# Performance work log

Measured on AMD Instinct MI355X. Metric: run time of the kernel, lower is better.

The kernel has to match this reference:

```python
import jax, jax.numpy as jnp
from jax import lax
import numpy as np

QMIN, QMAX = -127.0, 127.0
STRIDE = (1, 1)
PADDING = ((1, 1), (1, 1))
DILATION = (1, 1)
DN = ('NCHW', 'OIHW', 'NCHW')


def _quantize_x(x, scale_x):
    # symmetric static per-tensor int8 quantization
    return jnp.clip(jnp.round(x / scale_x), QMIN, QMAX)


def _quantize_w(w):
    # symmetric dynamic per-output-channel int8 quantization
    scale_w = jnp.max(jnp.abs(w), axis=(1, 2, 3), keepdims=True) / QMAX  # [O,1,1,1]
    q_w = jnp.clip(jnp.round(w / scale_w), QMIN, QMAX)
    return q_w, scale_w


def setup_inputs() -> dict:
    key = jax.random.key(0)
    kx, kw, kb = jax.random.split(key, 3)
    B, C, H, W = 32, 128, 56, 56
    O, kH, kW = 256, 3, 3
    x = jax.random.normal(kx, (B, C, H, W), jnp.float32)
    weight = jax.random.normal(kw, (O, C, kH, kW), jnp.float32) * 0.05
    bias = jax.random.normal(kb, (O,), jnp.float32)
    scale_x = jnp.asarray(0.02, jnp.float32)  # static per-tensor scale buffer
    # exact int8 product lookup table: lut[a+127, b+127] = a*b
    v = np.arange(-127, 128, dtype=np.int32)
    lut = jnp.asarray(v[:, None] * v[None, :])
    return {"x": x, "weight": weight, "bias": bias, "scale_x": scale_x, "lut": lut}


def reference(x, weight, bias, scale_x, lut):
    # lut holds the exact int8 product table, so bgemm_int8(q_x, q_w, lut) is an
    # exact integer GEMM; im2col + bGEMM == conv of quantized tensors.
    q_x = _quantize_x(x, scale_x)            # [B,C,H,W] integer-valued fp32
    q_w, scale_w = _quantize_w(weight)       # [O,C,kH,kW], [O,1,1,1]
    acc = lax.conv_general_dilated(
        q_x, q_w, STRIDE, PADDING, rhs_dilation=DILATION, dimension_numbers=DN
    )                                        # [B,O,OH,OW] integer-valued accumulator
    out = acc * scale_x * scale_w.reshape(1, -1, 1, 1)  # per-channel dequant
    return out + bias.reshape(1, -1, 1, 1)
```

## Files before the change

### kernel.cpp

```cpp
#include <hip/hip_runtime.h>


#define BATCH 32
#define CIN   128
#define HH    56
#define WW    56
#define OCH   256

typedef __attribute__((ext_vector_type(4))) int int4v;
typedef __attribute__((ext_vector_type(2))) long longx2;

#define QX_BYTES (32 * 56 * 56 * 128)
#define QW_BYTES (256 * 1152)
#define WS_NEEDED (QX_BYTES + QW_BYTES + 1024)

__device__ __forceinline__ void gload_lds16(const void* g, void* l) {
  __builtin_amdgcn_global_load_lds(
      (const __attribute__((address_space(1))) unsigned int*)g,
      (__attribute__((address_space(3))) unsigned int*)l, 16, 0, 0);
}

__global__ __launch_bounds__(256) void quant_w_kernel(
    const float* __restrict__ w, const float* __restrict__ sxp,
    char* __restrict__ qwf, float* __restrict__ alpha) {
  __shared__ float wf[1152];
  __shared__ float red[256];
  const int o = blockIdx.x;
  const int tid = threadIdx.x;
  const float* wrow = w + (size_t)o * 1152;
  float m = 0.f;
  for (int i = tid; i < 288; i += 256) {
    const float4 v = ((const float4*)wrow)[i];
    ((float4*)wf)[i] = v;
    m = fmaxf(m, fmaxf(fmaxf(fabsf(v.x), fabsf(v.y)),
                       fmaxf(fabsf(v.z), fabsf(v.w))));
  }
  red[tid] = m;
  __syncthreads();
  for (int s = 128; s > 0; s >>= 1) {
    if (tid < s) red[tid] = fmaxf(red[tid], red[tid + s]);
    __syncthreads();
  }
  const float sc = red[0] / 127.0f;
  if (tid == 0) alpha[o] = sc * sxp[0];
  if (tid < 36) {
    const int r = tid >> 2, c04 = tid & 3;
    const int og = o >> 5, t = (o >> 4) & 1, l16 = o & 15;
    unsigned int* base = (unsigned int*)(qwf + (size_t)og * 36864 +
                                         (size_t)(r * 4 + c04) * 1024);
#pragma unroll
    for (int quad = 0; quad < 4; ++quad) {
#pragma unroll
      for (int half = 0; half < 2; ++half) {
        unsigned int pk = 0;
#pragma unroll
        for (int k = 0; k < 4; ++k) {
          const int c = c04 * 32 + quad * 8 + half * 4 + k;
          const int q =
              (int)fminf(127.f, fmaxf(-127.f, rintf(wf[c * 9 + r] / sc)));
          pk |= ((unsigned int)(q & 255)) << (8 * k);
        }
        base[(l16 * 4 + quad) * 4 + t * 2 + half] = pk;
      }
    }
  }
}

__global__ __launch_bounds__(256) void quant_x_kernel(
    const float* __restrict__ x, const float* __restrict__ sxp,
    unsigned int* __restrict__ qxp) {
  __shared__ char ldsA[128 * 60];
  const int row = blockIdx.x;
  const int b = row / 56, h = row % 56;
  const float sx = sxp[0];
  for (int i = threadIdx.x; i < 1792; i += 256) {
    const int c = i / 14, f = i % 14;
    const float4 v =
        *(const float4*)(x + (((size_t)b * 128 + c) * 56 + h) * 56 + 4 * f);
    unsigned int pk;
    pk  = (unsigned int)((int)fminf(127.f, fmaxf(-127.f, rintf(v.x / sx))) & 255);
    pk |= ((unsigned int)((int)fminf(127.f, fmaxf(-127.f, rintf(v.y / sx))) & 255)) << 8;
    pk |= ((unsigned int)((int)fminf(127.f, fmaxf(-127.f, rintf(v.z / sx))) & 255)) << 16;
    pk |= ((unsigned int)((int)fminf(127.f, fmaxf(-127.f, rintf(v.w / sx))) & 255)) << 24;
    *(unsigned int*)(ldsA + c * 60 + 4 * f) = pk;
  }
  __syncthreads();
  unsigned int* orow = qxp + (size_t)row * 56 * 32;
  for (int i = threadIdx.x; i < 1792; i += 256) {
    const int w = i >> 5, jd = i & 31;
    const int c0 = (jd ^ (((w + 1) & 15) << 1)) << 2;
    unsigned int pk = 0;
#pragma unroll
    for (int k = 0; k < 4; ++k)
      pk |= ((unsigned int)(unsigned char)ldsA[(c0 + k) * 60 + w]) << (8 * k);
    orow[i] = pk;
  }
}

#define XSLAB 8448

__global__ __launch_bounds__(256, 4) void conv_kernel(
    const char* __restrict__ qxp, const char* __restrict__ qwf,
    const float* __restrict__ alpha, const float* __restrict__ bias,
    float* __restrict__ out) {
  __shared__ __attribute__((aligned(16))) char Xs8[3 * XSLAB];

  const int id = blockIdx.x;
  const int xcd = id & 7;
  int kk = id >> 3;
  const int yy = (kk >= 224) ? 1 : 0;
  kk -= yy * 224;
  const int bi = xcd * 224 + kk;
  const int b  = bi / 56;
  const int oh = bi % 56;
  const int o0 = yy * 128;
  const int tid = threadIdx.x;
  const int wave = tid >> 6, lane = tid & 63;
  const int l16 = lane & 15, quad = lane >> 4;

  int m_r[4], n_r[4];
  {
    int4v zz = {0, 0, 0, 0};
    long a1 = 0, b1 = 0, a2 = 0, b2 = 0;
    if (quad == 0) {
      a1 = 1L;
      b1 = (long)(l16 + 1);
      a2 = (long)(l16 + 1);
      b2 = 1L;
    }
    int4v d1 = __builtin_amdgcn_mfma_i32_16x16x32_i8(a1, b1, zz, 0, 0, 0);
    int4v d2 = __builtin_amdgcn_mfma_i32_16x16x32_i8(a2, b2, zz, 0, 0, 0);
#pragma unroll
    for (int r = 0; r < 4; ++r) {
      n_r[r] = (d1[r] - 1) & 15;
      m_r[r] = (d2[r] - 1) & 15;
    }
  }

  const longx2* wb2 = (const longx2*)(qwf + (size_t)(yy * 4 + wave) * 36864) +
                      (l16 * 4 + quad);
  longx2 ap[2][4];
#pragma unroll
  for (int c04 = 0; c04 < 4; ++c04) ap[0][c04] = wb2[(size_t)c04 * 64];

  for (int kh = 0; kh < 3; ++kh) {
    const int ih = oh - 1 + kh;
    char* slab = Xs8 + kh * XSLAB;
    if (ih >= 0 && ih < HH) {
      const char* src = qxp + ((size_t)b * 56 + ih) * 7168;
      for (int i = tid; i < 448; i += 256)
        gload_lds16(src + i * 16, slab + 128 + i * 16);
      for (int i = tid; i < 320; i += 256) {
        const int cg = i >> 5, dw = i & 31;
        const int col = (cg == 0) ? 0 : 56 + cg;
        ((unsigned int*)slab)[col * 32 + dw] = 0u;
      }
    } else {
      for (int i = tid; i < 2112; i += 256) ((unsigned int*)slab)[i] = 0u;
    }
  }

  int4v acc[2][4];
#pragma unroll
  for (int t = 0; t < 2; ++t)
#pragma unroll
    for (int u = 0; u < 4; ++u) acc[t][u] = (int4v){0, 0, 0, 0};

  __syncthreads();

  long bops[2][4];
  {
    const int ph0 = (l16 & 15) << 3;
    const int boff0 = (quad * 8) ^ ph0;
#pragma unroll
    for (int u = 0; u < 4; ++u)
      bops[0][u] = *(const long*)(Xs8 + (u * 16 + l16) * 128 + boff0);
  }
#pragma unroll
  for (int step = 0; step < 36; ++step) {
    const int g = step >> 2, c04 = step & 3;
    if (step + 1 < 36) {
      const int gn = (step + 1) >> 2, cn = (step + 1) & 3;
      const int khn = gn / 3, kwn = gn % 3;
      const char* Xkn = Xs8 + khn * XSLAB;
      const int phn = ((l16 + kwn) & 15) << 3;
      const int boffn = (cn * 32 + quad * 8) ^ phn;
#pragma unroll
      for (int u = 0; u < 4; ++u)
        bops[(step + 1) & 1][u] =
            *(const long*)(Xkn + (u * 16 + l16 + kwn) * 128 + boffn);
    }
    if (c04 == 0 && g < 8) {
#pragma unroll
      for (int cc = 0; cc < 4; ++cc)
        ap[(g + 1) & 1][cc] = wb2[(size_t)((g + 1) * 4 + cc) * 64];
    }
#pragma unroll
    for (int u = 0; u < 4; ++u) {
      acc[0][u] = __builtin_amdgcn_mfma_i32_16x16x32_i8(
          ap[g & 1][c04][0], bops[step & 1][u], acc[0][u], 0, 0, 0);
      acc[1][u] = __builtin_amdgcn_mfma_i32_16x16x32_i8(
          ap[g & 1][c04][1], bops[step & 1][u], acc[1][u], 0, 0, 0);
    }
  }

#pragma unroll
  for (int t = 0; t < 2; ++t) {
#pragma unroll
    for (int u = 0; u < 4; ++u) {
#pragma unroll
      for (int r = 0; r < 4; ++r) {
        const int ol = wave * 32 + t * 16 + m_r[r];
        const int ow = u * 16 + n_r[r];
        if (ow < WW) {
          const int oo = o0 + ol;
          out[(((size_t)b * OCH + oo) * HH + oh) * WW + ow] =
              (float)acc[t][u][r] * alpha[oo] + bias[oo];
        }
      }
    }
  }
}

#define FAS_ROW 392
#define FXS_ROW 136
#define FLDS_XS (128 * FAS_ROW)
#define FLDS_SC (FLDS_XS + 66 * FXS_ROW)
#define FLDS_AL (FLDS_SC + 512)
#define FLDS_BI (FLDS_AL + 512)
#define FLDS_RED (FLDS_BI + 512)
#define FLDS_TOT (FLDS_RED + 1024)

__global__ __launch_bounds__(256) void conv_fused_kernel(
    const float* __restrict__ x, const float* __restrict__ w,
    const float* __restrict__ bias, const float* __restrict__ sxp,
    float* __restrict__ out) {
  __shared__ __attribute__((aligned(16))) char lds[FLDS_TOT];
  char* As8 = lds;
  char* Xs8 = lds + FLDS_XS;
  float* scaleS = (float*)(lds + FLDS_SC);
  float* alphaS = (float*)(lds + FLDS_AL);
  float* biasS  = (float*)(lds + FLDS_BI);
  float* red    = (float*)(lds + FLDS_RED);

  const int bi = blockIdx.x;
  const int b  = bi / 56;
  const int oh = bi % 56;
  const int o0 = blockIdx.y * 128;
  const int tid = threadIdx.x;
  const int wave = tid >> 6, lane = tid & 63;
  const int l16 = lane & 15, quad = lane >> 4;
  const float sx = sxp[0];

  int m_r[4], n_r[4];
  {
    int4v zz = {0, 0, 0, 0};
    long a1 = 0, b1 = 0, a2 = 0, b2 = 0;
    if (quad == 0) { a1 = 1L; b1 = (long)(l16 + 1); a2 = (long)(l16 + 1); b2 = 1L; }
    int4v d1 = __builtin_amdgcn_mfma_i32_16x16x32_i8(a1, b1, zz, 0, 0, 0);
    int4v d2 = __builtin_amdgcn_mfma_i32_16x16x32_i8(a2, b2, zz, 0, 0, 0);
#pragma unroll
    for (int r = 0; r < 4; ++r) { n_r[r] = (d1[r] - 1) & 15; m_r[r] = (d2[r] - 1) & 15; }
  }
  {
    const int o = tid >> 1, half = tid & 1;
    const float4* p = (const float4*)(w + (size_t)(o0 + o) * 1152 + half * 576);
    float m = 0.f;
#pragma unroll 4
    for (int i = 0; i < 144; ++i) {
      const float4 v = p[i];
      m = fmaxf(m, fmaxf(fmaxf(fabsf(v.x), fabsf(v.y)), fmaxf(fabsf(v.z), fabsf(v.w))));
    }
    red[tid] = m;
  }
  __syncthreads();
  {
    const int o = tid >> 1;
    if ((tid & 1) == 0) {
      const float sc = fmaxf(red[2 * o], red[2 * o + 1]) / 127.0f;
      scaleS[o] = sc; alphaS[o] = sc * sx; biasS[o] = bias[o0 + o];
    }
  }
  int4v acc[2][4];
#pragma unroll
  for (int t = 0; t < 2; ++t)
#pragma unroll
    for (int u = 0; u < 4; ++u) acc[t][u] = (int4v){0, 0, 0, 0};

  for (int kh = 0; kh < 3; ++kh) {
    const int ih = oh - 1 + kh;
    const bool row_ok = (ih >= 0) && (ih < HH);
    __syncthreads();
    for (int idx = tid; idx < 66 * 128; idx += 256) {
      const int col = idx % 66, c = idx / 66, iw = col - 1;
      int q = 0;
      if (row_ok && iw >= 0 && iw < WW) {
        const float xv = x[(((size_t)b * CIN + c) * HH + ih) * WW + iw];
        q = (int)fminf(127.f, fmaxf(-127.f, rintf(xv / sx)));
      }
      Xs8[col * FXS_ROW + c] = (char)q;
    }
    for (int idx = tid; idx < 16384; idx += 256) {
      const int c = idx & 127, o = idx >> 7;
      const float s = scaleS[o];
      const float* wp = w + (size_t)(o0 + o) * 1152 + c * 9 + kh * 3;
#pragma unroll
      for (int kw = 0; kw < 3; ++kw) {
        const int q = (int)fminf(127.f, fmaxf(-127.f, rintf(wp[kw] / s)));
        As8[o * FAS_ROW + kw * 128 + c] = (char)q;
      }
    }
    __syncthreads();
    const int obase = wave * 32;
#pragma unroll
    for (int kw = 0; kw < 3; ++kw) {
#pragma unroll
      for (int c0 = 0; c0 < 128; c0 += 32) {
        long aop[2], bop[4];
#pragma unroll
        for (int t = 0; t < 2; ++t)
          aop[t] = *(const long*)(As8 + (obase + t * 16 + l16) * FAS_ROW + kw * 128 + c0 + quad * 8);
#pragma unroll
        for (int u = 0; u < 4; ++u)
          bop[u] = *(const long*)(Xs8 + (u * 16 + l16 + kw) * FXS_ROW + c0 + quad * 8);
#pragma unroll
        for (int t = 0; t < 2; ++t)
#pragma unroll
          for (int u = 0; u < 4; ++u)
            acc[t][u] = __builtin_amdgcn_mfma_i32_16x16x32_i8(aop[t], bop[u], acc[t][u], 0, 0, 0);
      }
    }
  }
#pragma unroll
  for (int t = 0; t < 2; ++t) {
#pragma unroll
    for (int u = 0; u < 4; ++u) {
#pragma unroll
      for (int r = 0; r < 4; ++r) {
        const int ol = wave * 32 + t * 16 + m_r[r];
        const int ow = u * 16 + n_r[r];
        if (ow < WW)
          out[(((size_t)b * OCH + o0 + ol) * HH + oh) * WW + ow] =
              (float)acc[t][u][r] * alphaS[ol] + biasS[ol];
      }
    }
  }
}

extern "C" void kernel_launch(void* const* d_in, const int* in_sizes, int n_in,
                              void* d_out, int out_size, void* d_ws, size_t ws_size,
                              hipStream_t stream) {
  const float *x = nullptr, *w = nullptr, *bias = nullptr, *sx = nullptr;
  for (int i = 0; i < n_in; ++i) {
    const int s = in_sizes[i];
    if (s == BATCH * CIN * HH * WW) x = (const float*)d_in[i];
    else if (s == OCH * CIN * 9)    w = (const float*)d_in[i];
    else if (s == OCH)              bias = (const float*)d_in[i];
    else if (s == 1)                sx = (const float*)d_in[i];
  }
  if (!x || !w || !bias || !sx) {
    x = (const float*)d_in[0]; w = (const float*)d_in[1];
    bias = (const float*)d_in[2]; sx = (const float*)d_in[3];
  }
  float* out = (float*)d_out;

  if (ws_size >= (size_t)WS_NEEDED) {
    unsigned int* qxp = (unsigned int*)d_ws;
    char* qwf = (char*)d_ws + QX_BYTES;
    float* alpha = (float*)((char*)d_ws + QX_BYTES + QW_BYTES);
    quant_w_kernel<<<OCH, 256, 0, stream>>>(w, sx, qwf, alpha);
    quant_x_kernel<<<BATCH * HH, 256, 0, stream>>>(x, sx, qxp);
    conv_kernel<<<BATCH * HH * 2, 256, 0, stream>>>(
        (const char*)qxp, qwf, alpha, bias, out);
  } else {
    conv_fused_kernel<<<dim3(BATCH * HH, 2), 256, 0, stream>>>(x, w, bias, sx, out);
  }
}
```

Measured before the change: 191.0 us.

## Compute two output rows per conv block to reuse weights and input slabs

Each conv block now produces two adjacent output rows instead of one. It loads four input rows into LDS (instead of three per row) and applies each weight fragment to both rows, so weight global loads and LDS input staging are shared across rows. The grid is halved and per-thread accumulators double, which raises register pressure and may lower occupancy under the 4-block launch bound. The MFMA-based lane-index probe is replaced by a direct formula (row = quad*4+r, column = l16), with alpha and bias loaded once per output channel.

```diff
diff --git a/kernel.cpp b/kernel.cpp
--- a/kernel.cpp
+++ b/kernel.cpp
@@ -103,49 +103,30 @@
     const char* __restrict__ qxp, const char* __restrict__ qwf,
     const float* __restrict__ alpha, const float* __restrict__ bias,
     float* __restrict__ out) {
-  __shared__ __attribute__((aligned(16))) char Xs8[3 * XSLAB];
+  __shared__ __attribute__((aligned(16))) char Xs8[4 * XSLAB];
 
   const int id = blockIdx.x;
   const int xcd = id & 7;
   int kk = id >> 3;
-  const int yy = (kk >= 224) ? 1 : 0;
-  kk -= yy * 224;
-  const int bi = xcd * 224 + kk;
-  const int b  = bi / 56;
-  const int oh = bi % 56;
+  const int yy = (kk >= 112) ? 1 : 0;
+  kk -= yy * 112;
+  const int bi2 = xcd * 112 + kk;
+  const int b  = bi2 / 28;
+  const int oh0 = (bi2 % 28) * 2;
   const int o0 = yy * 128;
   const int tid = threadIdx.x;
   const int wave = tid >> 6, lane = tid & 63;
   const int l16 = lane & 15, quad = lane >> 4;
 
-  int m_r[4], n_r[4];
-  {
-    int4v zz = {0, 0, 0, 0};
-    long a1 = 0, b1 = 0, a2 = 0, b2 = 0;
-    if (quad == 0) {
-      a1 = 1L;
-      b1 = (long)(l16 + 1);
-      a2 = (long)(l16 + 1);
-      b2 = 1L;
-    }
-    int4v d1 = __builtin_amdgcn_mfma_i32_16x16x32_i8(a1, b1, zz, 0, 0, 0);
-    int4v d2 = __builtin_amdgcn_mfma_i32_16x16x32_i8(a2, b2, zz, 0, 0, 0);
-#pragma unroll
-    for (int r = 0; r < 4; ++r) {
-      n_r[r] = (d1[r] - 1) & 15;
-      m_r[r] = (d2[r] - 1) & 15;
-    }
-  }
-
   const longx2* wb2 = (const longx2*)(qwf + (size_t)(yy * 4 + wave) * 36864) +
                       (l16 * 4 + quad);
   longx2 ap[2][4];
 #pragma unroll
   for (int c04 = 0; c04 < 4; ++c04) ap[0][c04] = wb2[(size_t)c04 * 64];
 
-  for (int kh = 0; kh < 3; ++kh) {
-    const int ih = oh - 1 + kh;
-    char* slab = Xs8 + kh * XSLAB;
+  for (int s = 0; s < 4; ++s) {
+    const int ih = oh0 - 1 + s;
+    char* slab = Xs8 + s * XSLAB;
     if (ih >= 0 && ih < HH) {
       const char* src = qxp + ((size_t)b * 56 + ih) * 7168;
       for (int i = tid; i < 448; i += 256)
@@ -160,21 +141,26 @@
     }
   }
 
-  int4v acc[2][4];
-#pragma unroll
-  for (int t = 0; t < 2; ++t)
-#pragma unroll
-    for (int u = 0; u < 4; ++u) acc[t][u] = (int4v){0, 0, 0, 0};
+  int4v acc[2][2][4];
+#pragma unroll
+  for (int p = 0; p < 2; ++p)
+#pragma unroll
+    for (int t = 0; t < 2; ++t)
+#pragma unroll
+      for (int u = 0; u < 4; ++u) acc[p][t][u] = (int4v){0, 0, 0, 0};
 
   __syncthreads();
 
-  long bops[2][4];
+  long bops[2][2][4];
   {
     const int ph0 = (l16 & 15) << 3;
     const int boff0 = (quad * 8) ^ ph0;
 #pragma unroll
-    for (int u = 0; u < 4; ++u)
-      bops[0][u] = *(const long*)(Xs8 + (u * 16 + l16) * 128 + boff0);
+    for (int p = 0; p < 2; ++p)
+#pragma unroll
+      for (int u = 0; u < 4; ++u)
+        bops[0][p][u] =
+            *(const long*)(Xs8 + p * XSLAB + (u * 16 + l16) * 128 + boff0);
   }
 #pragma unroll
   for (int step = 0; step < 36; ++step) {
@@ -182,13 +168,15 @@
     if (step + 1 < 36) {
       const int gn = (step + 1) >> 2, cn = (step + 1) & 3;
       const int khn = gn / 3, kwn = gn % 3;
-      const char* Xkn = Xs8 + khn * XSLAB;
       const int phn = ((l16 + kwn) & 15) << 3;
       const int boffn = (cn * 32 + quad * 8) ^ phn;
 #pragma unroll
-      for (int u = 0; u < 4; ++u)
-        bops[(step + 1) & 1][u] =
-            *(const long*)(Xkn + (u * 16 + l16 + kwn) * 128 + boffn);
+      for (int p = 0; p < 2; ++p)
+#pragma unroll
+        for (int u = 0; u < 4; ++u)
+          bops[(step + 1) & 1][p][u] =
+              *(const long*)(Xs8 + (khn + p) * XSLAB +
+                             (u * 16 + l16 + kwn) * 128 + boffn);
     }
     if (c04 == 0 && g < 8) {
 #pragma unroll
@@ -196,26 +184,29 @@
         ap[(g + 1) & 1][cc] = wb2[(size_t)((g + 1) * 4 + cc) * 64];
     }
 #pragma unroll
-    for (int u = 0; u < 4; ++u) {
-      acc[0][u] = __builtin_amdgcn_mfma_i32_16x16x32_i8(
-          ap[g & 1][c04][0], bops[step & 1][u], acc[0][u], 0, 0, 0);
-      acc[1][u] = __builtin_amdgcn_mfma_i32_16x16x32_i8(
-          ap[g & 1][c04][1], bops[step & 1][u], acc[1][u], 0, 0, 0);
-    }
+    for (int p = 0; p < 2; ++p)
+#pragma unroll
+      for (int u = 0; u < 4; ++u) {
+        acc[p][0][u] = __builtin_amdgcn_mfma_i32_16x16x32_i8(
+            ap[g & 1][c04][0], bops[step & 1][p][u], acc[p][0][u], 0, 0, 0);
+        acc[p][1][u] = __builtin_amdgcn_mfma_i32_16x16x32_i8(
+            ap[g & 1][c04][1], bops[step & 1][p][u], acc[p][1][u], 0, 0, 0);
+      }
   }
 
 #pragma unroll
   for (int t = 0; t < 2; ++t) {
 #pragma unroll
-    for (int u = 0; u < 4; ++u) {
-#pragma unroll
-      for (int r = 0; r < 4; ++r) {
-        const int ol = wave * 32 + t * 16 + m_r[r];
-        const int ow = u * 16 + n_r[r];
-        if (ow < WW) {
-          const int oo = o0 + ol;
-          out[(((size_t)b * OCH + oo) * HH + oh) * WW + ow] =
-              (float)acc[t][u][r] * alpha[oo] + bias[oo];
+    for (int r = 0; r < 4; ++r) {
+      const int o = o0 + wave * 32 + t * 16 + quad * 4 + r;
+      const float al = alpha[o], bz = bias[o];
+#pragma unroll
+      for (int p = 0; p < 2; ++p) {
+        float* orow = out + (((size_t)b * OCH + o) * HH + oh0 + p) * WW;
+#pragma unroll
+        for (int u = 0; u < 4; ++u) {
+          const int ow = u * 16 + l16;
+          if (ow < WW) orow[ow] = (float)acc[p][t][u][r] * al + bz;
         }
       }
     }
@@ -370,7 +361,7 @@
     float* alpha = (float*)((char*)d_ws + QX_BYTES + QW_BYTES);
     quant_w_kernel<<<OCH, 256, 0, stream>>>(w, sx, qwf, alpha);
     quant_x_kernel<<<BATCH * HH, 256, 0, stream>>>(x, sx, qxp);
-    conv_kernel<<<BATCH * HH * 2, 256, 0, stream>>>(
+    conv_kernel<<<BATCH * HH, 256, 0, stream>>>(
         (const char*)qxp, qwf, alpha, bias, out);
   } else {
     conv_fused_kernel<<<dim3(BATCH * HH, 2), 256, 0, stream>>>(x, w, bias, sx, out);
```

Measured after the change: 291.4 us. 1.53x slower.

## Merge both output-channel halves into one 512-thread block per output row

Applied to the files above, without the earlier changes.

The conv kernel now launches one 512-thread block per (batch, output row) instead of two 256-thread blocks split by output-channel half, so each input slab is staged into shared memory once and reused by all 256 output channels. The MFMA-based probe that derived output row/column lane mappings is replaced by a hardcoded mapping (quad*4+r rows, l16 columns), and the epilogue hoists alpha/bias loads per channel. The trade-offs are half as many blocks, larger blocks that may limit occupancy under the stated launch bounds, and reliance on the assumed MFMA output layout.

```diff
diff --git a/kernel.cpp b/kernel.cpp
--- a/kernel.cpp
+++ b/kernel.cpp
@@ -99,7 +99,7 @@
 
 #define XSLAB 8448
 
-__global__ __launch_bounds__(256, 4) void conv_kernel(
+__global__ __launch_bounds__(512, 4) void conv_kernel(
     const char* __restrict__ qxp, const char* __restrict__ qwf,
     const float* __restrict__ alpha, const float* __restrict__ bias,
     float* __restrict__ out) {
@@ -107,37 +107,14 @@
 
   const int id = blockIdx.x;
   const int xcd = id & 7;
-  int kk = id >> 3;
-  const int yy = (kk >= 224) ? 1 : 0;
-  kk -= yy * 224;
-  const int bi = xcd * 224 + kk;
+  const int bi = xcd * 224 + (id >> 3);
   const int b  = bi / 56;
   const int oh = bi % 56;
-  const int o0 = yy * 128;
   const int tid = threadIdx.x;
   const int wave = tid >> 6, lane = tid & 63;
   const int l16 = lane & 15, quad = lane >> 4;
 
-  int m_r[4], n_r[4];
-  {
-    int4v zz = {0, 0, 0, 0};
-    long a1 = 0, b1 = 0, a2 = 0, b2 = 0;
-    if (quad == 0) {
-      a1 = 1L;
-      b1 = (long)(l16 + 1);
-      a2 = (long)(l16 + 1);
-      b2 = 1L;
-    }
-    int4v d1 = __builtin_amdgcn_mfma_i32_16x16x32_i8(a1, b1, zz, 0, 0, 0);
-    int4v d2 = __builtin_amdgcn_mfma_i32_16x16x32_i8(a2, b2, zz, 0, 0, 0);
-#pragma unroll
-    for (int r = 0; r < 4; ++r) {
-      n_r[r] = (d1[r] - 1) & 15;
-      m_r[r] = (d2[r] - 1) & 15;
-    }
-  }
-
-  const longx2* wb2 = (const longx2*)(qwf + (size_t)(yy * 4 + wave) * 36864) +
+  const longx2* wb2 = (const longx2*)(qwf + (size_t)wave * 36864) +
                       (l16 * 4 + quad);
   longx2 ap[2][4];
 #pragma unroll
@@ -148,15 +125,14 @@
     char* slab = Xs8 + kh * XSLAB;
     if (ih >= 0 && ih < HH) {
       const char* src = qxp + ((size_t)b * 56 + ih) * 7168;
-      for (int i = tid; i < 448; i += 256)
-        gload_lds16(src + i * 16, slab + 128 + i * 16);
-      for (int i = tid; i < 320; i += 256) {
+      if (tid < 448) gload_lds16(src + tid * 16, slab + 128 + tid * 16);
+      for (int i = tid; i < 320; i += 512) {
         const int cg = i >> 5, dw = i & 31;
         const int col = (cg == 0) ? 0 : 56 + cg;
         ((unsigned int*)slab)[col * 32 + dw] = 0u;
       }
     } else {
-      for (int i = tid; i < 2112; i += 256) ((unsigned int*)slab)[i] = 0u;
+      for (int i = tid; i < 2112; i += 512) ((unsigned int*)slab)[i] = 0u;
     }
   }
 
@@ -207,16 +183,14 @@
 #pragma unroll
   for (int t = 0; t < 2; ++t) {
 #pragma unroll
-    for (int u = 0; u < 4; ++u) {
-#pragma unroll
-      for (int r = 0; r < 4; ++r) {
-        const int ol = wave * 32 + t * 16 + m_r[r];
-        const int ow = u * 16 + n_r[r];
-        if (ow < WW) {
-          const int oo = o0 + ol;
-          out[(((size_t)b * OCH + oo) * HH + oh) * WW + ow] =
-              (float)acc[t][u][r] * alpha[oo] + bias[oo];
-        }
+    for (int r = 0; r < 4; ++r) {
+      const int o = wave * 32 + t * 16 + quad * 4 + r;
+      const float al = alpha[o], bz = bias[o];
+      float* orow = out + (((size_t)b * OCH + o) * HH + oh) * WW;
+#pragma unroll
+      for (int u = 0; u < 4; ++u) {
+        const int ow = u * 16 + l16;
+        if (ow < WW) orow[ow] = (float)acc[t][u][r] * al + bz;
       }
     }
   }
@@ -370,7 +344,7 @@
     float* alpha = (float*)((char*)d_ws + QX_BYTES + QW_BYTES);
     quant_w_kernel<<<OCH, 256, 0, stream>>>(w, sx, qwf, alpha);
     quant_x_kernel<<<BATCH * HH, 256, 0, stream>>>(x, sx, qxp);
-    conv_kernel<<<BATCH * HH * 2, 256, 0, stream>>>(
+    conv_kernel<<<BATCH * HH, 512, 0, stream>>>(
         (const char*)qxp, qwf, alpha, bias, out);
   } else {
     conv_fused_kernel<<<dim3(BATCH * HH, 2), 256, 0, stream>>>(x, w, bias, sx, out);
```

Result: no change. 189.7 us (-0.7%).
